# Performance work log

Hardware: AMD Instinct MI355X
Metric: run time of the kernel (lower is better)

## Reference

```python
import jax, jax.numpy as jnp
import numpy as np

B, S, D = 4, 2048, 1024
E = 8
H = int(D * 2.5)  # 2560


def setup_inputs() -> dict:
    key = jax.random.key(0)
    ks = jax.random.split(key, 6)
    scale = 0.02
    x = jax.random.normal(ks[0], (B, S, D), dtype=jnp.float32)
    Wr = jax.random.normal(ks[1], (E, D), dtype=jnp.float32) * scale   # router: logits = x @ Wr.T
    Wg = jax.random.normal(ks[2], (E, H, D), dtype=jnp.float32) * scale  # gate proj per expert
    Wu = jax.random.normal(ks[3], (E, H, D), dtype=jnp.float32) * scale  # up proj per expert
    Wd = jax.random.normal(ks[4], (E, D, H), dtype=jnp.float32) * scale  # down proj per expert
    return {"x": x, "Wr": Wr, "Wg": Wg, "Wu": Wu, "Wd": Wd, "top_k": 2}


def reference(x, Wr, Wg, Wu, Wd, top_k):
    num_experts = Wg.shape[0]
    logits = jnp.einsum('bsd,ed->bse', x, Wr)              # [B,S,E]
    probs = jax.nn.softmax(logits, axis=-1)
    k = min(top_k, num_experts)
    topv, topi = jax.lax.top_k(probs, k)                   # [B,S,k]
    out = jnp.zeros_like(x)
    for ei in range(num_experts):
        mask = jnp.any(topi == ei, axis=-1)                # [B,S] bool
        h = jax.nn.silu(jnp.einsum('bsd,hd->bsh', x, Wg[ei])) \
            * jnp.einsum('bsd,hd->bsh', x, Wu[ei])         # [B,S,H]
        ex = jnp.einsum('bsh,dh->bsd', h, Wd[ei])          # [B,S,D]
        w = (probs[..., ei] * mask.astype(x.dtype))[..., None]
        out = out + ex * w
    return (out, logits, probs, topi)
```

## Files before the change

kernel.cpp:

```cpp
#include <hip/hip_runtime.h>

#define T_TOK 8192
#define DD    1024
#define EE    8
#define HH    2560
#define PAIR_CAP (T_TOK*2 + 128)
#define MT_MAX 64
#define NT1   (HH/64)
#define NT2   (DD/128)

typedef __attribute__((ext_vector_type(8))) short bf16x8;
typedef __attribute__((ext_vector_type(4))) float f32x4;

__device__ __forceinline__ unsigned short f2b(float f) {
  union { float f; unsigned u; } v; v.f = f;
  unsigned r = v.u + 0x7FFFu + ((v.u >> 16) & 1u);
  return (unsigned short)(r >> 16);
}

__device__ __forceinline__ void async16(const void* g, void* l) {
  __builtin_amdgcn_global_load_lds(
      (const __attribute__((address_space(1))) unsigned int*)(unsigned long long)g,
      (__attribute__((address_space(3))) unsigned int*)l,
      16, 0, 0);
}

__global__ void zero_ints(int* a, int n) {
  int i = threadIdx.x;
  if (i < n) a[i] = 0;
}

__global__ void conv_bf16_3(const float* __restrict__ s0, const float* __restrict__ s1,
                            const float* __restrict__ s2,
                            unsigned short* __restrict__ d0, unsigned short* __restrict__ d1,
                            unsigned short* __restrict__ d2, int n4) {
  int i = blockIdx.x * blockDim.x + threadIdx.x;
  if (i >= n4) return;
  const float* s = (blockIdx.y == 0) ? s0 : (blockIdx.y == 1) ? s1 : s2;
  unsigned short* d = (blockIdx.y == 0) ? d0 : (blockIdx.y == 1) ? d1 : d2;
  float4 v = ((const float4*)s)[i];
  ushort4 o;
  o.x = f2b(v.x); o.y = f2b(v.y); o.z = f2b(v.z); o.w = f2b(v.w);
  ((ushort4*)d)[i] = o;
}

__global__ __launch_bounds__(256) void router(
    const float* __restrict__ x, const float* __restrict__ Wr,
    unsigned short* __restrict__ xb,
    float* __restrict__ o_logits, float* __restrict__ o_probs, float* __restrict__ o_topi,
    int* __restrict__ top_e, float* __restrict__ top_p, int* __restrict__ counts)
{
  __shared__ float sWr[EE * DD];
  int tid = threadIdx.x;
  const float4* w4 = (const float4*)Wr;
  float4* s4 = (float4*)sWr;
  for (int i = tid; i < EE * DD / 4; i += 256) s4[i] = w4[i];
  __syncthreads();

  int wv = tid >> 6, lane = tid & 63;
  int t = blockIdx.x * 4 + wv;
  const float4* xt4 = (const float4*)(x + (size_t)t * DD);
  ushort4* xbt = (ushort4*)(xb + (size_t)t * DD);

  float acc[EE];
#pragma unroll
  for (int e = 0; e < EE; e++) acc[e] = 0.f;
#pragma unroll
  for (int p = 0; p < 4; p++) {
    float4 v = xt4[p * 64 + lane];
    ushort4 o;
    o.x = f2b(v.x); o.y = f2b(v.y); o.z = f2b(v.z); o.w = f2b(v.w);
    xbt[p * 64 + lane] = o;
    int d = (p * 64 + lane) * 4;
#pragma unroll
    for (int e = 0; e < EE; e++) {
      const float* wr = &sWr[e * DD + d];
      acc[e] += v.x * wr[0] + v.y * wr[1] + v.z * wr[2] + v.w * wr[3];
    }
  }
#pragma unroll
  for (int e = 0; e < EE; e++) {
#pragma unroll
    for (int off = 32; off; off >>= 1) acc[e] += __shfl_down(acc[e], off);
  }
  if (lane == 0) {
    float mx = acc[0];
#pragma unroll
    for (int e = 1; e < EE; e++) mx = fmaxf(mx, acc[e]);
    float p[EE]; float sum = 0.f;
#pragma unroll
    for (int e = 0; e < EE; e++) { p[e] = __expf(acc[e] - mx); sum += p[e]; }
    float inv = 1.f / sum;
#pragma unroll
    for (int e = 0; e < EE; e++) {
      p[e] *= inv;
      o_logits[(size_t)t * EE + e] = acc[e];
      o_probs [(size_t)t * EE + e] = p[e];
    }
    int i0 = 0;
#pragma unroll
    for (int e = 1; e < EE; e++) if (p[e] > p[i0]) i0 = e;
    int i1 = (i0 == 0) ? 1 : 0;
#pragma unroll
    for (int e = 0; e < EE; e++) if (e != i0 && p[e] > p[i1]) i1 = e;

    o_topi[t * 2 + 0] = (float)i0;
    o_topi[t * 2 + 1] = (float)i1;
    top_e[t * 2 + 0] = i0; top_e[t * 2 + 1] = i1;
    top_p[t * 2 + 0] = p[i0]; top_p[t * 2 + 1] = p[i1];
    atomicAdd(&counts[i0], 1);
    atomicAdd(&counts[i1], 1);
  }
}

__global__ void mk_offsets(const int* __restrict__ counts, int* __restrict__ offsets,
                           int* __restrict__ cursors) {
  if (threadIdx.x == 0) {
    int s = 0;
    for (int e = 0; e < EE; e++) { offsets[e] = s; s += counts[e]; }
  }
  if (threadIdx.x < EE) cursors[threadIdx.x] = 0;
}

__global__ void scatter(const int* __restrict__ top_e,
                        const int* __restrict__ offsets, int* __restrict__ cursors,
                        int* __restrict__ list, int* __restrict__ slot) {
  int t = blockIdx.x * blockDim.x + threadIdx.x;
  if (t >= T_TOK) return;
#pragma unroll
  for (int k = 0; k < 2; k++) {
    int e = top_e[t * 2 + k];
    int pos = atomicAdd(&cursors[e], 1);
    int dst = offsets[e] + pos;
    list[dst] = t;
    slot[t * 2 + k] = dst;
  }
}

__global__ __launch_bounds__(256) void gemm_gateup(
    const unsigned short* __restrict__ xb,
    const unsigned short* __restrict__ Wgb,
    const unsigned short* __restrict__ Wub,
    const int* __restrict__ list, const int* __restrict__ offsets,
    const int* __restrict__ counts,
    unsigned short* __restrict__ hbuf)
{
  int bx = blockIdx.x;
  int e = bx / (MT_MAX * NT1);
  int rem = bx - e * (MT_MAX * NT1);
  int mt = rem / NT1;
  int nt = rem - mt * NT1;
  int n_e = counts[e];
  if (mt * 128 >= n_e) return;
  int off_e = offsets[e];

  __shared__ unsigned short sA [2][128 * 32];
  __shared__ unsigned short sBg[2][ 64 * 32];
  __shared__ unsigned short sBu[2][ 64 * 32];

  int tid = threadIdx.x, wv = tid >> 6, lane = tid & 63;
  const unsigned short* wg_e = Wgb + (size_t)e * HH * DD;
  const unsigned short* wu_e = Wub + (size_t)e * HH * DD;

  size_t aBase[2];
#pragma unroll
  for (int i = 0; i < 2; i++) {
    int c = i * 256 + tid;
    int r = c >> 2, j = c & 3;
    int jj = j ^ ((r >> 1) & 3);
    int idx = mt * 128 + r;
    if (idx >= n_e) idx = n_e - 1;
    int tok = list[off_e + idx];
    aBase[i] = (size_t)tok * DD + (size_t)(jj * 8);
  }
  size_t bBase;
  {
    int r = tid >> 2, j = tid & 3;
    int jj = j ^ ((r >> 1) & 3);
    bBase = (size_t)(nt * 64 + r) * DD + (size_t)(jj * 8);
  }

  f32x4 accg[4][2] = {};
  f32x4 accu[4][2] = {};
  int wm = (wv >> 1) * 64, wn = (wv & 1) * 32;

  auto stage = [&](int b, int k0) {
    async16(xb  + aBase[0] + k0, &sA [b][(      wv * 64) * 8]);
    async16(xb  + aBase[1] + k0, &sA [b][(256 + wv * 64) * 8]);
    async16(wg_e + bBase   + k0, &sBg[b][(      wv * 64) * 8]);
    async16(wu_e + bBase   + k0, &sBu[b][(      wv * 64) * 8]);
  };

  const int NK = DD / 32;
  stage(0, 0);
  stage(1, 32);
  int q = lane >> 4;
  for (int t = 0; t < NK; ++t) {
    int cur = t & 1;
    if (t == NK - 1) asm volatile("s_waitcnt vmcnt(0)" ::: "memory");
    else             asm volatile("s_waitcnt vmcnt(4)" ::: "memory");
    __builtin_amdgcn_s_barrier();

    bf16x8 af[4], bg[2], bu[2];
#pragma unroll
    for (int fi = 0; fi < 4; fi++) {
      int r = wm + fi * 16 + (lane & 15);
      int ch = q ^ ((r >> 1) & 3);
      af[fi] = *(const bf16x8*)&sA[cur][r * 32 + ch * 8];
    }
#pragma unroll
    for (int fj = 0; fj < 2; fj++) {
      int r = wn + fj * 16 + (lane & 15);
      int ch = q ^ ((r >> 1) & 3);
      bg[fj] = *(const bf16x8*)&sBg[cur][r * 32 + ch * 8];
      bu[fj] = *(const bf16x8*)&sBu[cur][r * 32 + ch * 8];
    }
    asm volatile("s_waitcnt lgkmcnt(0)" ::: "memory");
    __builtin_amdgcn_sched_barrier(0);
    __builtin_amdgcn_s_barrier();
    if (t + 2 < NK) stage(cur, (t + 2) * 32);

    __builtin_amdgcn_s_setprio(1);
#pragma unroll
    for (int fi = 0; fi < 4; fi++)
#pragma unroll
      for (int fj = 0; fj < 2; fj++) {
        accg[fi][fj] = __builtin_amdgcn_mfma_f32_16x16x32_bf16(af[fi], bg[fj], accg[fi][fj], 0, 0, 0);
        accu[fi][fj] = __builtin_amdgcn_mfma_f32_16x16x32_bf16(af[fi], bu[fj], accu[fi][fj], 0, 0, 0);
      }
    __builtin_amdgcn_s_setprio(0);
  }

#pragma unroll
  for (int fi = 0; fi < 4; fi++) {
    int mBase = mt * 128 + wm + fi * 16 + ((lane >> 4) << 2);
#pragma unroll
    for (int fj = 0; fj < 2; fj++) {
      int col = nt * 64 + wn + fj * 16 + (lane & 15);
#pragma unroll
      for (int r = 0; r < 4; r++) {
        int m = mBase + r;
        if (m < n_e) {
          float g = accg[fi][fj][r];
          float u = accu[fi][fj][r];
          float hv = g / (1.f + __expf(-g)) * u;
          hbuf[(size_t)(off_e + m) * HH + col] = f2b(hv);
        }
      }
    }
  }
}

__global__ __launch_bounds__(256) void gemm_down(
    const unsigned short* __restrict__ hbuf,
    const unsigned short* __restrict__ Wdb,
    const int* __restrict__ offsets,
    const int* __restrict__ counts,
    float* __restrict__ tmp)
{
  int bx = blockIdx.x;
  int e = bx / (MT_MAX * NT2);
  int rem = bx - e * (MT_MAX * NT2);
  int mt = rem / NT2;
  int nt = rem - mt * NT2;
  int n_e = counts[e];
  if (mt * 128 >= n_e) return;
  int off_e = offsets[e];

  __shared__ unsigned short sA[2][128 * 32];
  __shared__ unsigned short sB[2][128 * 32];
  int tid = threadIdx.x, wv = tid >> 6, lane = tid & 63;
  const unsigned short* wd_e = Wdb + (size_t)e * DD * HH;

  size_t aBase[2], bBase[2];
#pragma unroll
  for (int i = 0; i < 2; i++) {
    int c = i * 256 + tid;
    int r = c >> 2, j = c & 3;
    int jj = j ^ ((r >> 1) & 3);
    aBase[i] = (size_t)(off_e + mt * 128 + r) * HH + (size_t)(jj * 8);
    bBase[i] = (size_t)(nt * 128 + r) * HH + (size_t)(jj * 8);
  }

  f32x4 acc[4][4] = {};
  int wm = (wv >> 1) * 64, wn = (wv & 1) * 64;

  auto stage = [&](int b, int k0) {
    async16(hbuf + aBase[0] + k0, &sA[b][(      wv * 64) * 8]);
    async16(hbuf + aBase[1] + k0, &sA[b][(256 + wv * 64) * 8]);
    async16(wd_e + bBase[0] + k0, &sB[b][(      wv * 64) * 8]);
    async16(wd_e + bBase[1] + k0, &sB[b][(256 + wv * 64) * 8]);
  };

  const int NK = HH / 32;
  stage(0, 0);
  stage(1, 32);
  int q = lane >> 4;
  for (int t = 0; t < NK; ++t) {
    int cur = t & 1;
    if (t == NK - 1) asm volatile("s_waitcnt vmcnt(0)" ::: "memory");
    else             asm volatile("s_waitcnt vmcnt(4)" ::: "memory");
    __builtin_amdgcn_s_barrier();

    bf16x8 af[4], bfr[4];
#pragma unroll
    for (int f = 0; f < 4; f++) {
      int ra = wm + f * 16 + (lane & 15);
      int ca = q ^ ((ra >> 1) & 3);
      af[f] = *(const bf16x8*)&sA[cur][ra * 32 + ca * 8];
      int rb = wn + f * 16 + (lane & 15);
      int cb = q ^ ((rb >> 1) & 3);
      bfr[f] = *(const bf16x8*)&sB[cur][rb * 32 + cb * 8];
    }
    asm volatile("s_waitcnt lgkmcnt(0)" ::: "memory");
    __builtin_amdgcn_sched_barrier(0);
    __builtin_amdgcn_s_barrier();
    if (t + 2 < NK) stage(cur, (t + 2) * 32);

    __builtin_amdgcn_s_setprio(1);
#pragma unroll
    for (int fi = 0; fi < 4; fi++)
#pragma unroll
      for (int fj = 0; fj < 4; fj++)
        acc[fi][fj] = __builtin_amdgcn_mfma_f32_16x16x32_bf16(af[fi], bfr[fj], acc[fi][fj], 0, 0, 0);
    __builtin_amdgcn_s_setprio(0);
  }

#pragma unroll
  for (int fi = 0; fi < 4; fi++) {
    int mBase = mt * 128 + wm + fi * 16 + ((lane >> 4) << 2);
#pragma unroll
    for (int r = 0; r < 4; r++) {
      int m = mBase + r;
      if (m < n_e) {
        float* orow = tmp + (size_t)(off_e + m) * DD + nt * 128 + wn;
#pragma unroll
        for (int fj = 0; fj < 4; fj++)
          orow[fj * 16 + (lane & 15)] = acc[fi][fj][r];
      }
    }
  }
}

__global__ __launch_bounds__(256) void combine(
    const float* __restrict__ tmp, const int* __restrict__ slot,
    const float* __restrict__ top_p, float* __restrict__ out)
{
  int t = blockIdx.x, d = threadIdx.x;
  int s0 = slot[t * 2 + 0], s1 = slot[t * 2 + 1];
  float p0 = top_p[t * 2 + 0], p1 = top_p[t * 2 + 1];
  float4 a = ((const float4*)(tmp + (size_t)s0 * DD))[d];
  float4 b = ((const float4*)(tmp + (size_t)s1 * DD))[d];
  float4 o;
  o.x = p0 * a.x + p1 * b.x;
  o.y = p0 * a.y + p1 * b.y;
  o.z = p0 * a.z + p1 * b.z;
  o.w = p0 * a.w + p1 * b.w;
  ((float4*)(out + (size_t)t * DD))[d] = o;
}

extern "C" void kernel_launch(void* const* d_in, const int* in_sizes, int n_in,
                              void* d_out, int out_size, void* d_ws, size_t ws_size,
                              hipStream_t stream) {
  const float* x  = (const float*)d_in[0];
  const float* Wr = (const float*)d_in[1];
  const float* Wg = (const float*)d_in[2];
  const float* Wu = (const float*)d_in[3];
  const float* Wd = (const float*)d_in[4];

  float* out      = (float*)d_out;
  float* o_logits = out + (size_t)T_TOK * DD;
  float* o_probs  = o_logits + (size_t)T_TOK * EE;
  float* o_topi   = o_probs + (size_t)T_TOK * EE;

  char* w = (char*)d_ws;
  auto alloc = [&](size_t bytes) {
    char* p = w;
    w += (bytes + 255) & ~(size_t)255;
    return p;
  };
  unsigned short* Wgb = (unsigned short*)alloc((size_t)EE * HH * DD * 2);
  unsigned short* Wub = (unsigned short*)alloc((size_t)EE * HH * DD * 2);
  unsigned short* Wdb = (unsigned short*)alloc((size_t)EE * DD * HH * 2);
  unsigned short* xb  = (unsigned short*)alloc((size_t)T_TOK * DD * 2);
  unsigned short* hb  = (unsigned short*)alloc((size_t)PAIR_CAP * HH * 2);
  int*   top_e   = (int*)  alloc((size_t)T_TOK * 2 * 4);
  float* top_p   = (float*)alloc((size_t)T_TOK * 2 * 4);
  int*   counts  = (int*)  alloc(64);
  int*   offsets = (int*)  alloc(64);
  int*   cursors = (int*)  alloc(64);
  int*   list    = (int*)  alloc((size_t)PAIR_CAP * 4);
  int*   slot    = (int*)  alloc((size_t)T_TOK * 2 * 4);

  float* tmp = (float*)Wgb;

  zero_ints<<<1, 64, 0, stream>>>(counts, EE);
  {
    int nw4 = EE * HH * DD / 4;
    dim3 g((nw4 + 255) / 256, 3);
    conv_bf16_3<<<g, 256, 0, stream>>>(Wg, Wu, Wd, Wgb, Wub, Wdb, nw4);
  }
  router<<<T_TOK / 4, 256, 0, stream>>>(x, Wr, xb, o_logits, o_probs, o_topi, top_e, top_p, counts);
  mk_offsets<<<1, 64, 0, stream>>>(counts, offsets, cursors);
  scatter<<<T_TOK / 256, 256, 0, stream>>>(top_e, offsets, cursors, list, slot);
  gemm_gateup<<<EE * MT_MAX * NT1, 256, 0, stream>>>(xb, Wgb, Wub, list, offsets, counts, hb);
  gemm_down<<<EE * MT_MAX * NT2, 256, 0, stream>>>(hb, Wdb, offsets, counts, tmp);
  combine<<<T_TOK, 256, 0, stream>>>(tmp, slot, top_p, out);
}
```

Baseline: 899.4 us.

## Double N-tile width of both expert GEMMs, aggregate scatter atomics per wave

Gate/up GEMM tiles widen from 128x64 to 128x128 and the down GEMM from 128x128 to 128x256. Each block now computes more MFMAs per staged A tile, which cuts repeated loads of the gathered activations and the number of blocks. The scatter kernel replaces one atomic per token with a per-wave ballot that issues a single atomic per expert, and the counts zeroing is folded into the conversion kernel to save a launch. The cost is doubled accumulator registers and LDS per block, which can lower occupancy or cause spills, and fewer blocks for the GPU to balance across CUs.

```diff
diff --git a/kernel.cpp b/kernel.cpp
--- a/kernel.cpp
+++ b/kernel.cpp
@@ -6,8 +6,8 @@
 #define HH    2560
 #define PAIR_CAP (T_TOK*2 + 128)
 #define MT_MAX 64
-#define NT1   (HH/64)
-#define NT2   (DD/128)
+#define NT1B  (HH/128)
+#define NT2B  (DD/256)
 
 typedef __attribute__((ext_vector_type(8))) short bf16x8;
 typedef __attribute__((ext_vector_type(4))) float f32x4;
@@ -25,15 +25,11 @@
       16, 0, 0);
 }
 
-__global__ void zero_ints(int* a, int n) {
-  int i = threadIdx.x;
-  if (i < n) a[i] = 0;
-}
-
 __global__ void conv_bf16_3(const float* __restrict__ s0, const float* __restrict__ s1,
                             const float* __restrict__ s2,
                             unsigned short* __restrict__ d0, unsigned short* __restrict__ d1,
-                            unsigned short* __restrict__ d2, int n4) {
+                            unsigned short* __restrict__ d2, int n4, int* __restrict__ counts) {
+  if (blockIdx.x == 0 && blockIdx.y == 0 && threadIdx.x < EE) counts[threadIdx.x] = 0;
   int i = blockIdx.x * blockDim.x + threadIdx.x;
   if (i >= n4) return;
   const float* s = (blockIdx.y == 0) ? s0 : (blockIdx.y == 1) ? s1 : s2;
@@ -127,10 +123,24 @@
                         int* __restrict__ list, int* __restrict__ slot) {
   int t = blockIdx.x * blockDim.x + threadIdx.x;
   if (t >= T_TOK) return;
+  int lane = threadIdx.x & 63;
+  unsigned long long lower = (lane == 63) ? ~0ull >> 1 : (1ull << lane) - 1;
 #pragma unroll
   for (int k = 0; k < 2; k++) {
     int e = top_e[t * 2 + k];
-    int pos = atomicAdd(&cursors[e], 1);
+    int pos = 0;
+#pragma unroll
+    for (int ee = 0; ee < EE; ee++) {
+      unsigned long long m = __ballot(e == ee);
+      if (e == ee) {
+        int rank = __popcll(m & lower);
+        int base = 0;
+        if (rank == 0) base = atomicAdd(&cursors[ee], __popcll(m));
+        int src = __ffsll((long long)m) - 1;
+        base = __shfl(base, src);
+        pos = base + rank;
+      }
+    }
     int dst = offsets[e] + pos;
     list[dst] = t;
     slot[t * 2 + k] = dst;
@@ -146,23 +156,23 @@
     unsigned short* __restrict__ hbuf)
 {
   int bx = blockIdx.x;
-  int e = bx / (MT_MAX * NT1);
-  int rem = bx - e * (MT_MAX * NT1);
-  int mt = rem / NT1;
-  int nt = rem - mt * NT1;
+  int e = bx / (MT_MAX * NT1B);
+  int rem = bx - e * (MT_MAX * NT1B);
+  int mt = rem / NT1B;
+  int nt = rem - mt * NT1B;
   int n_e = counts[e];
   if (mt * 128 >= n_e) return;
   int off_e = offsets[e];
 
   __shared__ unsigned short sA [2][128 * 32];
-  __shared__ unsigned short sBg[2][ 64 * 32];
-  __shared__ unsigned short sBu[2][ 64 * 32];
+  __shared__ unsigned short sBg[2][128 * 32];
+  __shared__ unsigned short sBu[2][128 * 32];
 
   int tid = threadIdx.x, wv = tid >> 6, lane = tid & 63;
   const unsigned short* wg_e = Wgb + (size_t)e * HH * DD;
   const unsigned short* wu_e = Wub + (size_t)e * HH * DD;
 
-  size_t aBase[2];
+  size_t aBase[2], bBase[2];
 #pragma unroll
   for (int i = 0; i < 2; i++) {
     int c = i * 256 + tid;
@@ -172,23 +182,20 @@
     if (idx >= n_e) idx = n_e - 1;
     int tok = list[off_e + idx];
     aBase[i] = (size_t)tok * DD + (size_t)(jj * 8);
-  }
-  size_t bBase;
-  {
-    int r = tid >> 2, j = tid & 3;
-    int jj = j ^ ((r >> 1) & 3);
-    bBase = (size_t)(nt * 64 + r) * DD + (size_t)(jj * 8);
-  }
-
-  f32x4 accg[4][2] = {};
-  f32x4 accu[4][2] = {};
-  int wm = (wv >> 1) * 64, wn = (wv & 1) * 32;
+    bBase[i] = (size_t)(nt * 128 + r) * DD + (size_t)(jj * 8);
+  }
+
+  f32x4 accg[4][4] = {};
+  f32x4 accu[4][4] = {};
+  int wm = (wv >> 1) * 64, wn = (wv & 1) * 64;
 
   auto stage = [&](int b, int k0) {
-    async16(xb  + aBase[0] + k0, &sA [b][(      wv * 64) * 8]);
-    async16(xb  + aBase[1] + k0, &sA [b][(256 + wv * 64) * 8]);
-    async16(wg_e + bBase   + k0, &sBg[b][(      wv * 64) * 8]);
-    async16(wu_e + bBase   + k0, &sBu[b][(      wv * 64) * 8]);
+    async16(xb   + aBase[0] + k0, &sA [b][(      wv * 64) * 8]);
+    async16(xb   + aBase[1] + k0, &sA [b][(256 + wv * 64) * 8]);
+    async16(wg_e + bBase[0] + k0, &sBg[b][(      wv * 64) * 8]);
+    async16(wg_e + bBase[1] + k0, &sBg[b][(256 + wv * 64) * 8]);
+    async16(wu_e + bBase[0] + k0, &sBu[b][(      wv * 64) * 8]);
+    async16(wu_e + bBase[1] + k0, &sBu[b][(256 + wv * 64) * 8]);
   };
 
   const int NK = DD / 32;
@@ -198,22 +205,19 @@
   for (int t = 0; t < NK; ++t) {
     int cur = t & 1;
     if (t == NK - 1) asm volatile("s_waitcnt vmcnt(0)" ::: "memory");
-    else             asm volatile("s_waitcnt vmcnt(4)" ::: "memory");
+    else             asm volatile("s_waitcnt vmcnt(6)" ::: "memory");
     __builtin_amdgcn_s_barrier();
 
-    bf16x8 af[4], bg[2], bu[2];
-#pragma unroll
-    for (int fi = 0; fi < 4; fi++) {
-      int r = wm + fi * 16 + (lane & 15);
-      int ch = q ^ ((r >> 1) & 3);
-      af[fi] = *(const bf16x8*)&sA[cur][r * 32 + ch * 8];
-    }
-#pragma unroll
-    for (int fj = 0; fj < 2; fj++) {
-      int r = wn + fj * 16 + (lane & 15);
-      int ch = q ^ ((r >> 1) & 3);
-      bg[fj] = *(const bf16x8*)&sBg[cur][r * 32 + ch * 8];
-      bu[fj] = *(const bf16x8*)&sBu[cur][r * 32 + ch * 8];
+    bf16x8 af[4], bg[4], bu[4];
+#pragma unroll
+    for (int f = 0; f < 4; f++) {
+      int ra = wm + f * 16 + (lane & 15);
+      int ca = q ^ ((ra >> 1) & 3);
+      af[f] = *(const bf16x8*)&sA[cur][ra * 32 + ca * 8];
+      int rb = wn + f * 16 + (lane & 15);
+      int cb = q ^ ((rb >> 1) & 3);
+      bg[f] = *(const bf16x8*)&sBg[cur][rb * 32 + cb * 8];
+      bu[f] = *(const bf16x8*)&sBu[cur][rb * 32 + cb * 8];
     }
     asm volatile("s_waitcnt lgkmcnt(0)" ::: "memory");
     __builtin_amdgcn_sched_barrier(0);
@@ -224,7 +228,7 @@
 #pragma unroll
     for (int fi = 0; fi < 4; fi++)
 #pragma unroll
-      for (int fj = 0; fj < 2; fj++) {
+      for (int fj = 0; fj < 4; fj++) {
         accg[fi][fj] = __builtin_amdgcn_mfma_f32_16x16x32_bf16(af[fi], bg[fj], accg[fi][fj], 0, 0, 0);
         accu[fi][fj] = __builtin_amdgcn_mfma_f32_16x16x32_bf16(af[fi], bu[fj], accu[fi][fj], 0, 0, 0);
       }
@@ -235,8 +239,8 @@
   for (int fi = 0; fi < 4; fi++) {
     int mBase = mt * 128 + wm + fi * 16 + ((lane >> 4) << 2);
 #pragma unroll
-    for (int fj = 0; fj < 2; fj++) {
-      int col = nt * 64 + wn + fj * 16 + (lane & 15);
+    for (int fj = 0; fj < 4; fj++) {
+      int col = nt * 128 + wn + fj * 16 + (lane & 15);
 #pragma unroll
       for (int r = 0; r < 4; r++) {
         int m = mBase + r;
@@ -259,37 +263,44 @@
     float* __restrict__ tmp)
 {
   int bx = blockIdx.x;
-  int e = bx / (MT_MAX * NT2);
-  int rem = bx - e * (MT_MAX * NT2);
-  int mt = rem / NT2;
-  int nt = rem - mt * NT2;
+  int e = bx / (MT_MAX * NT2B);
+  int rem = bx - e * (MT_MAX * NT2B);
+  int mt = rem / NT2B;
+  int nt = rem - mt * NT2B;
   int n_e = counts[e];
   if (mt * 128 >= n_e) return;
   int off_e = offsets[e];
 
   __shared__ unsigned short sA[2][128 * 32];
-  __shared__ unsigned short sB[2][128 * 32];
+  __shared__ unsigned short sB[2][256 * 32];
   int tid = threadIdx.x, wv = tid >> 6, lane = tid & 63;
   const unsigned short* wd_e = Wdb + (size_t)e * DD * HH;
 
-  size_t aBase[2], bBase[2];
+  size_t aBase[2], bBase[4];
 #pragma unroll
   for (int i = 0; i < 2; i++) {
     int c = i * 256 + tid;
     int r = c >> 2, j = c & 3;
     int jj = j ^ ((r >> 1) & 3);
     aBase[i] = (size_t)(off_e + mt * 128 + r) * HH + (size_t)(jj * 8);
-    bBase[i] = (size_t)(nt * 128 + r) * HH + (size_t)(jj * 8);
-  }
-
-  f32x4 acc[4][4] = {};
-  int wm = (wv >> 1) * 64, wn = (wv & 1) * 64;
+  }
+#pragma unroll
+  for (int i = 0; i < 4; i++) {
+    int c = i * 256 + tid;
+    int r = c >> 2, j = c & 3;
+    int jj = j ^ ((r >> 1) & 3);
+    bBase[i] = (size_t)(nt * 256 + r) * HH + (size_t)(jj * 8);
+  }
+
+  f32x4 acc[4][8] = {};
+  int wm = (wv >> 1) * 64, wn = (wv & 1) * 128;
 
   auto stage = [&](int b, int k0) {
     async16(hbuf + aBase[0] + k0, &sA[b][(      wv * 64) * 8]);
     async16(hbuf + aBase[1] + k0, &sA[b][(256 + wv * 64) * 8]);
-    async16(wd_e + bBase[0] + k0, &sB[b][(      wv * 64) * 8]);
-    async16(wd_e + bBase[1] + k0, &sB[b][(256 + wv * 64) * 8]);
+#pragma unroll
+    for (int i = 0; i < 4; i++)
+      async16(wd_e + bBase[i] + k0, &sB[b][(i * 256 + wv * 64) * 8]);
   };
 
   const int NK = HH / 32;
@@ -299,15 +310,18 @@
   for (int t = 0; t < NK; ++t) {
     int cur = t & 1;
     if (t == NK - 1) asm volatile("s_waitcnt vmcnt(0)" ::: "memory");
-    else             asm volatile("s_waitcnt vmcnt(4)" ::: "memory");
+    else             asm volatile("s_waitcnt vmcnt(6)" ::: "memory");
     __builtin_amdgcn_s_barrier();
 
-    bf16x8 af[4], bfr[4];
+    bf16x8 af[4], bfr[8];
 #pragma unroll
     for (int f = 0; f < 4; f++) {
       int ra = wm + f * 16 + (lane & 15);
       int ca = q ^ ((ra >> 1) & 3);
       af[f] = *(const bf16x8*)&sA[cur][ra * 32 + ca * 8];
+    }
+#pragma unroll
+    for (int f = 0; f < 8; f++) {
       int rb = wn + f * 16 + (lane & 15);
       int cb = q ^ ((rb >> 1) & 3);
       bfr[f] = *(const bf16x8*)&sB[cur][rb * 32 + cb * 8];
@@ -321,7 +335,7 @@
 #pragma unroll
     for (int fi = 0; fi < 4; fi++)
 #pragma unroll
-      for (int fj = 0; fj < 4; fj++)
+      for (int fj = 0; fj < 8; fj++)
         acc[fi][fj] = __builtin_amdgcn_mfma_f32_16x16x32_bf16(af[fi], bfr[fj], acc[fi][fj], 0, 0, 0);
     __builtin_amdgcn_s_setprio(0);
   }
@@ -333,9 +347,9 @@
     for (int r = 0; r < 4; r++) {
       int m = mBase + r;
       if (m < n_e) {
-        float* orow = tmp + (size_t)(off_e + m) * DD + nt * 128 + wn;
-#pragma unroll
-        for (int fj = 0; fj < 4; fj++)
+        float* orow = tmp + (size_t)(off_e + m) * DD + nt * 256 + wn;
+#pragma unroll
+        for (int fj = 0; fj < 8; fj++)
           orow[fj * 16 + (lane & 15)] = acc[fi][fj][r];
       }
     }
@@ -394,16 +408,15 @@
 
   float* tmp = (float*)Wgb;
 
-  zero_ints<<<1, 64, 0, stream>>>(counts, EE);
   {
     int nw4 = EE * HH * DD / 4;
     dim3 g((nw4 + 255) / 256, 3);
-    conv_bf16_3<<<g, 256, 0, stream>>>(Wg, Wu, Wd, Wgb, Wub, Wdb, nw4);
+    conv_bf16_3<<<g, 256, 0, stream>>>(Wg, Wu, Wd, Wgb, Wub, Wdb, nw4, counts);
   }
   router<<<T_TOK / 4, 256, 0, stream>>>(x, Wr, xb, o_logits, o_probs, o_topi, top_e, top_p, counts);
   mk_offsets<<<1, 64, 0, stream>>>(counts, offsets, cursors);
   scatter<<<T_TOK / 256, 256, 0, stream>>>(top_e, offsets, cursors, list, slot);
-  gemm_gateup<<<EE * MT_MAX * NT1, 256, 0, stream>>>(xb, Wgb, Wub, list, offsets, counts, hb);
-  gemm_down<<<EE * MT_MAX * NT2, 256, 0, stream>>>(hb, Wdb, offsets, counts, tmp);
+  gemm_gateup<<<EE * MT_MAX * NT1B, 256, 0, stream>>>(xb, Wgb, Wub, list, offsets, counts, hb);
+  gemm_down<<<EE * MT_MAX * NT2B, 256, 0, stream>>>(hb, Wdb, offsets, counts, tmp);
   combine<<<T_TOK, 256, 0, stream>>>(tmp, slot, top_p, out);
 }
```

Result: slower. 1.070 ms (+18.9%).
